# Kernel tuning notes

Measured on AMD Instinct MI355X. Metric: run time of the kernel, lower is better.

Reference implementation:

```python
import jax, jax.numpy as jnp
import numpy as np

M, K, N, GROUP = 64, 4096, 11008, 128
NGROUPS = K // GROUP  # 32


def setup_inputs() -> dict:
    key = jax.random.key(0)
    k1, k2, k3, k4, k5 = jax.random.split(key, 5)
    x = jax.random.normal(k1, (M, K), dtype=jnp.float32)
    # packed int4 weights: 8 nibbles per int32, full 32-bit entropy
    qweight = jax.random.bits(k2, (K // 8, N), dtype=jnp.uint32).astype(jnp.int32)
    qzeros = jax.random.bits(k3, (NGROUPS, N // 8), dtype=jnp.uint32).astype(jnp.int32)
    scales = jax.random.uniform(k4, (NGROUPS, N), dtype=jnp.float32, minval=0.001, maxval=0.02)
    bias = jax.random.normal(k5, (N,), dtype=jnp.float32) * 0.01
    return {"x": x, "qweight": qweight, "qzeros": qzeros, "scales": scales, "bias": bias}


def dequantize(qweight, qzeros, scales):
    shifts = jnp.arange(8, dtype=jnp.int32) * 4  # nibble bit offsets 0..28
    # unpack weights: [K//8, N] -> [K//8, 8, N] -> [NGROUPS, GROUP, N]
    w = (jnp.right_shift(qweight[:, None, :], shifts[None, :, None]) & 15)
    w = w.reshape(-1, GROUP, qweight.shape[1])
    # unpack zeros: [NGROUPS, N//8] -> [NGROUPS, N//8, 8] -> [NGROUPS, 1, N]; GPTQ stores zero-1
    z = (jnp.right_shift(qzeros[:, :, None], shifts[None, None, :]) & 15) + 1
    z = z.reshape(z.shape[0], 1, -1)
    # scale * (q - zero), per group: [NGROUPS, GROUP, N] -> [K, N]
    W = scales[:, None, :] * (w - z).astype(scales.dtype)
    return W.reshape(-1, W.shape[2])


def reference(x, qweight, qzeros, scales, bias):
    W = dequantize(qweight, qzeros, scales)  # [K, N] fp32
    return jnp.matmul(x, W.astype(x.dtype)) + bias
```

## Files before the change

### kernel.cpp

```cpp
#include <hip/hip_runtime.h>
#include <hip/hip_bf16.h>

namespace {

constexpr int MM = 64;
constexpr int KK = 4096;
constexpr int NN = 11008;
constexpr int NZROW = NN / 8;
constexpr int BN = 128;
constexpr int KSPLIT = 8;
constexpr int KSEG = KK / KSPLIT;
constexpr int NTILES = NN / BN;
constexpr int BK = 32;
constexpr int NCH = KSEG / BK;
constexpr int RS = 20;
constexpr int ABUF = MM * RS;
constexpr int BBUF = BN * RS;
constexpr size_t WS_NEED = (size_t)KSPLIT * MM * NN * 4;

typedef float f32x4 __attribute__((ext_vector_type(4)));
typedef float f32x2 __attribute__((ext_vector_type(2)));
typedef short s16x8 __attribute__((ext_vector_type(8)));
typedef int   i32x4 __attribute__((ext_vector_type(4)));
typedef int   i32x2 __attribute__((ext_vector_type(2)));

__device__ __forceinline__ int pack_bf16(float a, float b) {
  union { __hip_bfloat162 h; int i; } u;
  u.h.x = __float2bfloat16(a);
  u.h.y = __float2bfloat16(b);
  return u.i;
}

__global__ __launch_bounds__(256) void prep_kernel(
    const float* __restrict__ bias, float* __restrict__ out)
{
  const int i = blockIdx.x * 256 + threadIdx.x;
  out[i] = bias[i % NN];
}

__global__ __launch_bounds__(256) void reduce_kernel(
    const float* __restrict__ ws, const float* __restrict__ bias,
    float* __restrict__ out)
{
  const int i4 = (blockIdx.x * 256 + threadIdx.x) * 4;
  f32x4 acc = *(const f32x4*)(bias + (i4 % NN));
  #pragma unroll
  for (int s = 0; s < KSPLIT; ++s)
    acc += *(const f32x4*)(ws + (size_t)s * (MM * NN) + i4);
  *(f32x4*)(out + i4) = acc;
}

template<bool ATOMIC>
__global__ __launch_bounds__(256, 4) void gptq_gemm_kernel(
    const float* __restrict__ x, const int* __restrict__ qw,
    const int* __restrict__ qz, const float* __restrict__ scales,
    float* __restrict__ out)
{
  __shared__ int As[2 * ABUF];
  __shared__ int Bs[2 * BBUF];

  const int tid  = threadIdx.x;
  const int wave = tid >> 6;
  const int lane = tid & 63;
  const int c    = lane & 15;
  const int quad = lane >> 4;

  const int ks     = blockIdx.x & 7;
  const int ntile  = blockIdx.x >> 3;
  const int n0     = ntile * BN;
  const int kbase0 = ks * KSEG;

  const int am   = tid >> 2;
  const int aseg = tid & 3;
  const int bu   = tid & 3;
  const int cp   = tid >> 2;
  const int Ncp  = n0 + 2 * cp;
  const int mrow = wave * 16 + quad * 4;

  const float* xrow = x + am * KK + aseg * 8;

  f32x4 acc[8];
  #pragma unroll
  for (int t = 0; t < 8; ++t) acc[t] = {0.f, 0.f, 0.f, 0.f};

  f32x4 pA0[2], pA1[2];
  f32x2 pS[2];
  int   pZ[2];
  i32x2 pB[3];

  auto pfA = [&](int i) {
    const int sl = i & 1;
    const int kc = kbase0 + i * BK;
    pA0[sl] = *(const f32x4*)(xrow + kc);
    pA1[sl] = *(const f32x4*)(xrow + kc + 4);
    const int g = kc >> 7;
    pS[sl] = *(const f32x2*)(scales + g * NN + Ncp);
    pZ[sl] = qz[g * NZROW + (Ncp >> 3)];
  };
  auto pfB = [&](int i) {
    const int kc = kbase0 + i * BK;
    pB[i % 3] = *(const i32x2*)(qw + (size_t)((kc >> 3) + bu) * NN + Ncp);
  };

  pfB(0); pfB(1); pfA(0);

  #pragma unroll
  for (int i = 0; i < NCH; ++i) {
    const int sl = i & 1;
    if (i + 2 < NCH) pfB(i + 2);
    if (i + 1 < NCH) pfA(i + 1);

    int* Abuf = As + sl * ABUF;
    i32x4 pa;
    pa.x = pack_bf16(pA0[sl].x, pA0[sl].y);
    pa.y = pack_bf16(pA0[sl].z, pA0[sl].w);
    pa.z = pack_bf16(pA1[sl].x, pA1[sl].y);
    pa.w = pack_bf16(pA1[sl].z, pA1[sl].w);
    *(i32x4*)&Abuf[am * RS + aseg * 4] = pa;

    int* Bbuf = Bs + sl * BBUF;
    const float s0 = pS[sl].x, s1 = pS[sl].y;
    const int sh0 = (Ncp & 7) * 4;
    const int z0  = (pZ[sl] >> sh0) & 15;
    const int z1  = (pZ[sl] >> (sh0 + 4)) & 15;
    const float C0 = (float)(0x800000 + z0 + 1);
    const float C1 = (float)(0x800000 + z1 + 1);
    const int v0 = pB[i % 3].x, v1 = pB[i % 3].y;
    i32x4 pb0, pb1;
    pb0.x = pack_bf16(s0 * (__int_as_float(((v0      ) & 15) | 0x4B000000) - C0),
                      s0 * (__int_as_float(((v0 >>  4) & 15) | 0x4B000000) - C0));
    pb0.y = pack_bf16(s0 * (__int_as_float(((v0 >>  8) & 15) | 0x4B000000) - C0),
                      s0 * (__int_as_float(((v0 >> 12) & 15) | 0x4B000000) - C0));
    pb0.z = pack_bf16(s0 * (__int_as_float(((v0 >> 16) & 15) | 0x4B000000) - C0),
                      s0 * (__int_as_float(((v0 >> 20) & 15) | 0x4B000000) - C0));
    pb0.w = pack_bf16(s0 * (__int_as_float(((v0 >> 24) & 15) | 0x4B000000) - C0),
                      s0 * (__int_as_float(((v0 >> 28) & 15) | 0x4B000000) - C0));
    pb1.x = pack_bf16(s1 * (__int_as_float(((v1      ) & 15) | 0x4B000000) - C1),
                      s1 * (__int_as_float(((v1 >>  4) & 15) | 0x4B000000) - C1));
    pb1.y = pack_bf16(s1 * (__int_as_float(((v1 >>  8) & 15) | 0x4B000000) - C1),
                      s1 * (__int_as_float(((v1 >> 12) & 15) | 0x4B000000) - C1));
    pb1.z = pack_bf16(s1 * (__int_as_float(((v1 >> 16) & 15) | 0x4B000000) - C1),
                      s1 * (__int_as_float(((v1 >> 20) & 15) | 0x4B000000) - C1));
    pb1.w = pack_bf16(s1 * (__int_as_float(((v1 >> 24) & 15) | 0x4B000000) - C1),
                      s1 * (__int_as_float(((v1 >> 28) & 15) | 0x4B000000) - C1));
    *(i32x4*)&Bbuf[(2 * cp    ) * RS + bu * 4] = pb0;
    *(i32x4*)&Bbuf[(2 * cp + 1) * RS + bu * 4] = pb1;

    __asm__ volatile("s_waitcnt lgkmcnt(0)\n\ts_barrier" ::: "memory");

    const s16x8 af = *(const s16x8*)&Abuf[(wave * 16 + c) * RS + quad * 4];
    #pragma unroll
    for (int t = 0; t < 8; ++t) {
      const s16x8 bfr = *(const s16x8*)&Bbuf[(t * 16 + c) * RS + quad * 4];
      acc[t] = __builtin_amdgcn_mfma_f32_16x16x32_bf16(af, bfr, acc[t], 0, 0, 0);
    }
  }

  if (ATOMIC) {
    #pragma unroll
    for (int t = 0; t < 8; ++t) {
      const int N = n0 + t * 16 + c;
      atomicAdd(&out[(mrow + 0) * NN + N], acc[t].x);
      atomicAdd(&out[(mrow + 1) * NN + N], acc[t].y);
      atomicAdd(&out[(mrow + 2) * NN + N], acc[t].z);
      atomicAdd(&out[(mrow + 3) * NN + N], acc[t].w);
    }
  } else {
    float* wsp = out + (size_t)ks * (MM * NN);
    #pragma unroll
    for (int t = 0; t < 8; ++t) {
      const int N = n0 + t * 16 + c;
      wsp[(mrow + 0) * NN + N] = acc[t].x;
      wsp[(mrow + 1) * NN + N] = acc[t].y;
      wsp[(mrow + 2) * NN + N] = acc[t].z;
      wsp[(mrow + 3) * NN + N] = acc[t].w;
    }
  }
}

}

extern "C" void kernel_launch(void* const* d_in, const int* in_sizes, int n_in,
                              void* d_out, int out_size, void* d_ws, size_t ws_size,
                              hipStream_t stream) {
  const float* x      = (const float*)d_in[0];
  const int*   qw     = (const int*)d_in[1];
  const int*   qz     = (const int*)d_in[2];
  const float* scales = (const float*)d_in[3];
  const float* bias   = (const float*)d_in[4];
  float* out = (float*)d_out;

  if (ws_size >= WS_NEED) {
    float* ws = (float*)d_ws;
    gptq_gemm_kernel<false><<<NTILES * KSPLIT, 256, 0, stream>>>(x, qw, qz, scales, ws);
    reduce_kernel<<<(MM * NN) / 1024, 256, 0, stream>>>(ws, bias, out);
  } else {
    prep_kernel<<<(MM * NN) / 256, 256, 0, stream>>>(bias, out);
    gptq_gemm_kernel<true><<<NTILES * KSPLIT, 256, 0, stream>>>(x, qw, qz, scales, out);
  }
}
```

Baseline: 97.72 us.

## Dequantize weights directly into MFMA registers and stage activations per quant group

Each wave now dequantizes its own 32 output columns of int4 weights straight into MFMA B-operand registers, removing the shared-memory round trip for B. Activations are staged into LDS once per 128-wide quant group instead of once per 32-wide chunk, so there is one barrier per four chunks instead of one per chunk. Scale and zero loads are likewise hoisted to once per group. In exchange, each wave holds more registers (eight prefetched activation vectors plus deeper weight prefetch), and the per-lane global weight loads become narrower scalar loads, which may reduce memory coalescing.

```diff
diff --git a/kernel.cpp b/kernel.cpp
--- a/kernel.cpp
+++ b/kernel.cpp
@@ -13,13 +13,15 @@
 constexpr int NTILES = NN / BN;
 constexpr int BK = 32;
 constexpr int NCH = KSEG / BK;
-constexpr int RS = 20;
-constexpr int ABUF = MM * RS;
-constexpr int BBUF = BN * RS;
+constexpr int GCH = 4;
+constexpr int NG = NCH / GCH;
+constexpr int AROWI = 68;
+constexpr int ABUFI = MM * AROWI;
 constexpr size_t WS_NEED = (size_t)KSPLIT * MM * NN * 4;
 
+static_assert(NCH % GCH == 0, "groups must tile chunks");
+
 typedef float f32x4 __attribute__((ext_vector_type(4)));
-typedef float f32x2 __attribute__((ext_vector_type(2)));
 typedef short s16x8 __attribute__((ext_vector_type(8)));
 typedef int   i32x4 __attribute__((ext_vector_type(4)));
 typedef int   i32x2 __attribute__((ext_vector_type(2)));
@@ -56,8 +58,7 @@
     const int* __restrict__ qz, const float* __restrict__ scales,
     float* __restrict__ out)
 {
-  __shared__ int As[2 * ABUF];
-  __shared__ int Bs[2 * BBUF];
+  __shared__ int As[2 * ABUFI];
 
   const int tid  = threadIdx.x;
   const int wave = tid >> 6;
@@ -69,111 +70,144 @@
   const int ntile  = blockIdx.x >> 3;
   const int n0     = ntile * BN;
   const int kbase0 = ks * KSEG;
-
-  const int am   = tid >> 2;
-  const int aseg = tid & 3;
-  const int bu   = tid & 3;
-  const int cp   = tid >> 2;
-  const int Ncp  = n0 + 2 * cp;
-  const int mrow = wave * 16 + quad * 4;
-
-  const float* xrow = x + am * KK + aseg * 8;
+  const int grp0   = kbase0 >> 7;
+
+  const int ncol = n0 + wave * 32 + c;
+
+  const int arow0 = wave * 16 + (lane >> 5);
+  const float* xp0 = x + (size_t)arow0 * KK + kbase0 + (lane & 31) * 4;
+
+  const int* qwb = qw + ((size_t)(kbase0 >> 3) + quad) * NN + ncol;
 
   f32x4 acc[8];
   #pragma unroll
   for (int t = 0; t < 8; ++t) acc[t] = {0.f, 0.f, 0.f, 0.f};
 
-  f32x4 pA0[2], pA1[2];
-  f32x2 pS[2];
-  int   pZ[2];
-  i32x2 pB[3];
-
-  auto pfA = [&](int i) {
-    const int sl = i & 1;
-    const int kc = kbase0 + i * BK;
-    pA0[sl] = *(const f32x4*)(xrow + kc);
-    pA1[sl] = *(const f32x4*)(xrow + kc + 4);
-    const int g = kc >> 7;
-    pS[sl] = *(const f32x2*)(scales + g * NN + Ncp);
-    pZ[sl] = qz[g * NZROW + (Ncp >> 3)];
+  f32x4 S[8];
+  int   pB0[4], pB1[4];
+  float pS0[2], pS1[2];
+  int   pZ0[2], pZ1[2];
+  float s0, s1, C0, C1;
+
+  auto stage_load = [&](int g) {
+    const float* xp = xp0 + g * 128;
+    #pragma unroll
+    for (int j = 0; j < 8; ++j)
+      S[j] = *(const f32x4*)(xp + (size_t)j * 2 * KK);
+  };
+  auto stage_write = [&](int g) {
+    int* Ab = As + (g & 1) * ABUFI + arow0 * AROWI + (lane & 31) * 2;
+    #pragma unroll
+    for (int j = 0; j < 8; ++j) {
+      i32x2 w2;
+      w2.x = pack_bf16(S[j].x, S[j].y);
+      w2.y = pack_bf16(S[j].z, S[j].w);
+      *(i32x2*)&Ab[j * 2 * AROWI] = w2;
+    }
   };
   auto pfB = [&](int i) {
-    const int kc = kbase0 + i * BK;
-    pB[i % 3] = *(const i32x2*)(qw + (size_t)((kc >> 3) + bu) * NN + Ncp);
-  };
-
-  pfB(0); pfB(1); pfA(0);
+    const int* qp = qwb + (size_t)i * 4 * NN;
+    pB0[i & 3] = qp[0];
+    pB1[i & 3] = qp[16];
+  };
+  auto pfS = [&](int g) {
+    const int sl = g & 1;
+    const float* sp = scales + (size_t)(grp0 + g) * NN + ncol;
+    pS0[sl] = sp[0];
+    pS1[sl] = sp[16];
+    const int* zp = qz + (size_t)(grp0 + g) * NZROW + (ncol >> 3);
+    pZ0[sl] = zp[0];
+    pZ1[sl] = zp[2];
+  };
+  auto setSC = [&](int g) {
+    const int sl = g & 1;
+    const int sh = (ncol & 7) * 4;
+    s0 = pS0[sl];
+    s1 = pS1[sl];
+    C0 = __int_as_float(0x4B000000 + ((pZ0[sl] >> sh) & 15) + 1);
+    C1 = __int_as_float(0x4B000000 + ((pZ1[sl] >> sh) & 15) + 1);
+  };
+  auto dq8 = [&](int v, float s, float C) -> i32x4 {
+    i32x4 p;
+    p.x = pack_bf16(s * (__int_as_float(((v      ) & 15) | 0x4B000000) - C),
+                    s * (__int_as_float(((v >>  4) & 15) | 0x4B000000) - C));
+    p.y = pack_bf16(s * (__int_as_float(((v >>  8) & 15) | 0x4B000000) - C),
+                    s * (__int_as_float(((v >> 12) & 15) | 0x4B000000) - C));
+    p.z = pack_bf16(s * (__int_as_float(((v >> 16) & 15) | 0x4B000000) - C),
+                    s * (__int_as_float(((v >> 20) & 15) | 0x4B000000) - C));
+    p.w = pack_bf16(s * (__int_as_float(((v >> 24) & 15) | 0x4B000000) - C),
+                    s * (__int_as_float(((v >> 28) & 15) | 0x4B000000) - C));
+    return p;
+  };
+
+  pfS(0);
+  stage_load(0);
+  pfB(0); pfB(1); pfB(2);
+  stage_write(0);
+  __asm__ volatile("s_waitcnt lgkmcnt(0)\n\ts_barrier" ::: "memory");
+  setSC(0);
+  pfS(1);
 
   #pragma unroll
   for (int i = 0; i < NCH; ++i) {
-    const int sl = i & 1;
-    if (i + 2 < NCH) pfB(i + 2);
-    if (i + 1 < NCH) pfA(i + 1);
-
-    int* Abuf = As + sl * ABUF;
-    i32x4 pa;
-    pa.x = pack_bf16(pA0[sl].x, pA0[sl].y);
-    pa.y = pack_bf16(pA0[sl].z, pA0[sl].w);
-    pa.z = pack_bf16(pA1[sl].x, pA1[sl].y);
-    pa.w = pack_bf16(pA1[sl].z, pA1[sl].w);
-    *(i32x4*)&Abuf[am * RS + aseg * 4] = pa;
-
-    int* Bbuf = Bs + sl * BBUF;
-    const float s0 = pS[sl].x, s1 = pS[sl].y;
-    const int sh0 = (Ncp & 7) * 4;
-    const int z0  = (pZ[sl] >> sh0) & 15;
-    const int z1  = (pZ[sl] >> (sh0 + 4)) & 15;
-    const float C0 = (float)(0x800000 + z0 + 1);
-    const float C1 = (float)(0x800000 + z1 + 1);
-    const int v0 = pB[i % 3].x, v1 = pB[i % 3].y;
-    i32x4 pb0, pb1;
-    pb0.x = pack_bf16(s0 * (__int_as_float(((v0      ) & 15) | 0x4B000000) - C0),
-                      s0 * (__int_as_float(((v0 >>  4) & 15) | 0x4B000000) - C0));
-    pb0.y = pack_bf16(s0 * (__int_as_float(((v0 >>  8) & 15) | 0x4B000000) - C0),
-                      s0 * (__int_as_float(((v0 >> 12) & 15) | 0x4B000000) - C0));
-    pb0.z = pack_bf16(s0 * (__int_as_float(((v0 >> 16) & 15) | 0x4B000000) - C0),
-                      s0 * (__int_as_float(((v0 >> 20) & 15) | 0x4B000000) - C0));
-    pb0.w = pack_bf16(s0 * (__int_as_float(((v0 >> 24) & 15) | 0x4B000000) - C0),
-                      s0 * (__int_as_float(((v0 >> 28) & 15) | 0x4B000000) - C0));
-    pb1.x = pack_bf16(s1 * (__int_as_float(((v1      ) & 15) | 0x4B000000) - C1),
-                      s1 * (__int_as_float(((v1 >>  4) & 15) | 0x4B000000) - C1));
-    pb1.y = pack_bf16(s1 * (__int_as_float(((v1 >>  8) & 15) | 0x4B000000) - C1),
-                      s1 * (__int_as_float(((v1 >> 12) & 15) | 0x4B000000) - C1));
-    pb1.z = pack_bf16(s1 * (__int_as_float(((v1 >> 16) & 15) | 0x4B000000) - C1),
-                      s1 * (__int_as_float(((v1 >> 20) & 15) | 0x4B000000) - C1));
-    pb1.w = pack_bf16(s1 * (__int_as_float(((v1 >> 24) & 15) | 0x4B000000) - C1),
-                      s1 * (__int_as_float(((v1 >> 28) & 15) | 0x4B000000) - C1));
-    *(i32x4*)&Bbuf[(2 * cp    ) * RS + bu * 4] = pb0;
-    *(i32x4*)&Bbuf[(2 * cp + 1) * RS + bu * 4] = pb1;
-
-    __asm__ volatile("s_waitcnt lgkmcnt(0)\n\ts_barrier" ::: "memory");
-
-    const s16x8 af = *(const s16x8*)&Abuf[(wave * 16 + c) * RS + quad * 4];
-    #pragma unroll
-    for (int t = 0; t < 8; ++t) {
-      const s16x8 bfr = *(const s16x8*)&Bbuf[(t * 16 + c) * RS + quad * 4];
-      acc[t] = __builtin_amdgcn_mfma_f32_16x16x32_bf16(af, bfr, acc[t], 0, 0, 0);
+    const int g = i >> 2, cc = i & 3, buf = g & 1;
+    if (cc == 0 && g + 1 < NG) stage_load(g + 1);
+    if (i + 3 < NCH) pfB(i + 3);
+
+    union { i32x4 i4; s16x8 s8; } u0, u1;
+    u0.i4 = dq8(pB0[i & 3], s0, C0);
+    u1.i4 = dq8(pB1[i & 3], s1, C1);
+
+    const int* Ab = As + buf * ABUFI;
+    const int aoff = c * AROWI + cc * 16 + quad * 4;
+    const s16x8 af0 = *(const s16x8*)&Ab[aoff];
+    const s16x8 af1 = *(const s16x8*)&Ab[aoff + 16 * AROWI];
+    const s16x8 af2 = *(const s16x8*)&Ab[aoff + 32 * AROWI];
+    const s16x8 af3 = *(const s16x8*)&Ab[aoff + 48 * AROWI];
+
+    acc[0] = __builtin_amdgcn_mfma_f32_16x16x32_bf16(af0, u0.s8, acc[0], 0, 0, 0);
+    acc[1] = __builtin_amdgcn_mfma_f32_16x16x32_bf16(af0, u1.s8, acc[1], 0, 0, 0);
+    acc[2] = __builtin_amdgcn_mfma_f32_16x16x32_bf16(af1, u0.s8, acc[2], 0, 0, 0);
+    acc[3] = __builtin_amdgcn_mfma_f32_16x16x32_bf16(af1, u1.s8, acc[3], 0, 0, 0);
+    acc[4] = __builtin_amdgcn_mfma_f32_16x16x32_bf16(af2, u0.s8, acc[4], 0, 0, 0);
+    acc[5] = __builtin_amdgcn_mfma_f32_16x16x32_bf16(af2, u1.s8, acc[5], 0, 0, 0);
+    acc[6] = __builtin_amdgcn_mfma_f32_16x16x32_bf16(af3, u0.s8, acc[6], 0, 0, 0);
+    acc[7] = __builtin_amdgcn_mfma_f32_16x16x32_bf16(af3, u1.s8, acc[7], 0, 0, 0);
+
+    if (cc == 3 && g + 1 < NG) {
+      stage_write(g + 1);
+      __asm__ volatile("s_waitcnt lgkmcnt(0)\n\ts_barrier" ::: "memory");
+      setSC(g + 1);
+      if (g + 2 < NG) pfS(g + 2);
     }
   }
 
   if (ATOMIC) {
     #pragma unroll
-    for (int t = 0; t < 8; ++t) {
-      const int N = n0 + t * 16 + c;
-      atomicAdd(&out[(mrow + 0) * NN + N], acc[t].x);
-      atomicAdd(&out[(mrow + 1) * NN + N], acc[t].y);
-      atomicAdd(&out[(mrow + 2) * NN + N], acc[t].z);
-      atomicAdd(&out[(mrow + 3) * NN + N], acc[t].w);
+    for (int r = 0; r < 4; ++r) {
+      #pragma unroll
+      for (int t = 0; t < 2; ++t) {
+        const f32x4 a = acc[r * 2 + t];
+        float* op = out + (size_t)(r * 16 + quad * 4) * NN + ncol + t * 16;
+        atomicAdd(&op[0],          a.x);
+        atomicAdd(&op[NN],         a.y);
+        atomicAdd(&op[2 * NN],     a.z);
+        atomicAdd(&op[3 * NN],     a.w);
+      }
     }
   } else {
     float* wsp = out + (size_t)ks * (MM * NN);
     #pragma unroll
-    for (int t = 0; t < 8; ++t) {
-      const int N = n0 + t * 16 + c;
-      wsp[(mrow + 0) * NN + N] = acc[t].x;
-      wsp[(mrow + 1) * NN + N] = acc[t].y;
-      wsp[(mrow + 2) * NN + N] = acc[t].z;
-      wsp[(mrow + 3) * NN + N] = acc[t].w;
+    for (int r = 0; r < 4; ++r) {
+      #pragma unroll
+      for (int t = 0; t < 2; ++t) {
+        const f32x4 a = acc[r * 2 + t];
+        float* op = wsp + (size_t)(r * 16 + quad * 4) * NN + ncol + t * 16;
+        op[0]      = a.x;
+        op[NN]     = a.y;
+        op[2 * NN] = a.z;
+        op[3 * NN] = a.w;
+      }
     }
   }
 }
```

After: 98.25 us. Within noise of the previous version (+0.5%).
